# Performance work log

Hardware: AMD Instinct MI355X
Metric: run time of the kernel (lower is better)

Reference implementation:

```python
import jax, jax.numpy as jnp
import numpy as np


def log_g(x):
    # Appendix B.3 of 'Were RNNs All We Needed?'
    return jnp.where(x >= 0, jnp.log(jax.nn.relu(x) + 0.5), -jax.nn.softplus(-x))


def parallel_scan_log(log_a, log_b):
    # h[0] = b[0]; h[i] = a[i]*h[i-1] + b[i], computed in log space along axis 1
    log_a_star = jnp.cumsum(log_a, axis=1)
    log_x0_plus_b_star = jax.lax.cumlogsumexp(log_b - log_a_star, axis=1)
    return jnp.exp(log_a_star + log_x0_plus_b_star)


def setup_inputs() -> dict:
    key = jax.random.key(0)
    B, T, D = 8, 4096, 1024
    k1, k2, k3, k4, k5 = jax.random.split(key, 5)
    scale = 1.0 / np.sqrt(D)
    return {
        "h_prev_layer": jax.random.normal(k1, (B, T, D), dtype=jnp.float32),
        "W_z": jax.random.uniform(k2, (D, D), jnp.float32, -scale, scale),
        "b_z": jax.random.uniform(k3, (D,), jnp.float32, -scale, scale),
        "W_h": jax.random.uniform(k4, (D, D), jnp.float32, -scale, scale),
        "b_h": jax.random.uniform(k5, (D,), jnp.float32, -scale, scale),
    }


def reference(h_prev_layer, W_z, b_z, W_h, b_h):
    k = jnp.einsum('btd,ed->bte', h_prev_layer, W_z) + b_z          # linear_z
    tilde_h = jnp.einsum('btd,ed->bte', h_prev_layer, W_h) + b_h    # linear_h
    log_z = -jax.nn.softplus(-k)
    log_one_minus_z = -jax.nn.softplus(k)
    log_tilde_h = log_g(tilde_h)
    return parallel_scan_log(log_one_minus_z, log_z + log_tilde_h)
```

## Files before the change

### kernel.cpp

```cpp
#include <hip/hip_runtime.h>
#include <hip/hip_fp16.h>

typedef float f32x4 __attribute__((ext_vector_type(4)));
typedef __bf16 bf16x8 __attribute__((ext_vector_type(8)));
typedef unsigned int u32x4 __attribute__((ext_vector_type(4)));
typedef __attribute__((address_space(3))) const void* lds_cp;

#define BB_ 8
#define TT_ 4096
#define DD_ 1024
#define MM_ (BB_*TT_)
#define KK_ DD_

#define NCH 64
#define LCH (TT_/NCH)

static __device__ __forceinline__ unsigned short f2bf_rn(float f) {
  unsigned int u = __float_as_uint(f);
  u += 0x7FFFu + ((u >> 16) & 1u);
  return (unsigned short)(u >> 16);
}

__global__ void cvt_f32_bf16(const float4* __restrict__ src,
                             ushort4* __restrict__ dst, int n4) {
  int stride = gridDim.x * blockDim.x;
  for (int i = blockIdx.x * blockDim.x + threadIdx.x; i < n4; i += stride) {
    float4 v = src[i];
    ushort4 o;
    o.x = f2bf_rn(v.x); o.y = f2bf_rn(v.y);
    o.z = f2bf_rn(v.z); o.w = f2bf_rn(v.w);
    dst[i] = o;
  }
}

__global__ void cvt_w(const float4* __restrict__ Wz4,
                      const float4* __restrict__ Wh4,
                      ushort4* __restrict__ Wcat) {
  int flat = blockIdx.x * 256 + threadIdx.x;
  int mtx = flat >> 18;
  int j = flat & 262143;
  float4 v = (mtx ? Wh4 : Wz4)[j];
  int D = j >> 8;
  int kq = j & 255;
  int e = ((D >> 5) << 6) + (mtx << 5) + (D & 31);
  ushort4 o;
  o.x = f2bf_rn(v.x); o.y = f2bf_rn(v.y);
  o.z = f2bf_rn(v.z); o.w = f2bf_rn(v.w);
  Wcat[(size_t)e * 256 + kq] = o;
}

__device__ __forceinline__ void gload_lds16(const void* g, void* l) {
  __builtin_amdgcn_global_load_lds(
      (const __attribute__((address_space(1))) void*)g,
      (__attribute__((address_space(3))) void*)l, 16, 0, 0);
}

#define STA(q, nb_, kkh) gload_lds16(pXa + (q) * 65536 + (kkh), (nb_) + (q) * 8192 + wofs)
#define STB(q, nb_, kkh) gload_lds16(pWb + (q) * 65536 + (kkh), (nb_) + 32768 + (q) * 8192 + wofs)

#define DSR(dst, gp) \
  asm volatile("ds_read_b128 %0, %1" : "=&v"(dst) : "v"((lds_cp)(gp)))

#define RD_A(SET, base_, mh, sk_) do {                                      \
    DSR(SET[0], (base_) + rA7 + (mh) * 8192 + 0 * 2048 + (sk_));            \
    DSR(SET[1], (base_) + rA7 + (mh) * 8192 + 1 * 2048 + (sk_));            \
    DSR(SET[2], (base_) + rA7 + (mh) * 8192 + 2 * 2048 + (sk_));            \
    DSR(SET[3], (base_) + rA7 + (mh) * 8192 + 3 * 2048 + (sk_));            \
  } while (0)
#define RD_B(SET, base_, sk_) do {                                          \
    DSR(SET[0], (base_) + rB7 + 0 * 2048 + (sk_));                          \
    DSR(SET[1], (base_) + rB7 + 1 * 2048 + (sk_));                          \
    DSR(SET[2], (base_) + rB7 + 2 * 2048 + (sk_));                          \
    DSR(SET[3], (base_) + rB7 + 3 * 2048 + (sk_));                          \
  } while (0)

#define BC(x) __builtin_bit_cast(bf16x8, x)
#define MFMA16(ASET, BSET, mh) do {                                         \
    __builtin_amdgcn_s_setprio(1);                                          \
    _Pragma("unroll")                                                       \
    for (int ii = 0; ii < 4; ++ii)                                          \
      _Pragma("unroll")                                                     \
      for (int j = 0; j < 4; ++j)                                           \
        acc[(mh) * 4 + ii][j] = __builtin_amdgcn_mfma_f32_16x16x32_bf16(    \
            BC(ASET[ii]), BC(BSET[j]), acc[(mh) * 4 + ii][j], 0, 0, 0);     \
    __builtin_amdgcn_s_setprio(0);                                          \
  } while (0)

#define BAR() do { __builtin_amdgcn_s_barrier();                            \
                   __builtin_amdgcn_sched_barrier(0); } while (0)
#define SB()  __builtin_amdgcn_sched_barrier(0)
#define LGKM(n) do { asm volatile("s_waitcnt lgkmcnt(" #n ")" ::: "memory");\
                     SB(); } while (0)
#define VMW(n) asm volatile("s_waitcnt vmcnt(" #n ")" ::: "memory")

__global__ __launch_bounds__(512, 2) void gemm_fused(
    const unsigned short* __restrict__ Xb,
    const unsigned short* __restrict__ Wb,
    const float* __restrict__ bz, const float* __restrict__ bh,
    unsigned int* __restrict__ ZG,
    float* __restrict__ Pp, float* __restrict__ Qq)
{
  extern __shared__ __align__(16) char smem[];
  const int tid  = threadIdx.x;
  const int wave = tid >> 6;
  const int lane = tid & 63;
  const int wm = wave >> 2, wn = wave & 3;
  const int fr = lane & 15, kg = lane >> 4;

  int swz = (blockIdx.x & 7) * 128 + (blockIdx.x >> 3);
  const int m0 = (swz >> 3) * 256;
  const int e0 = (swz & 7) * 256;

  const int arow = tid >> 3;
  const int aslx = ((tid & 7) ^ (arow & 7)) * 8;
  const unsigned short* pXa = Xb + (size_t)(m0 + arow) * KK_ + aslx;
  const unsigned short* pWb = Wb + (size_t)(e0 + arow) * KK_ + aslx;
  const int wofs = wave * 1024;

  const int rA7 = (wm * 128 + fr) * 128;
  const int rB7 = 32768 + (wn * 64 + fr) * 128;
  const int fx = fr & 7;
  const int sk0 = (kg ^ fx) * 16;
  const int sk1 = sk0 ^ 64;

  f32x4 acc[8][4];
  #pragma unroll
  for (int i = 0; i < 8; i++)
    #pragma unroll
    for (int j = 0; j < 4; j++)
      acc[i][j] = (f32x4){0.f, 0.f, 0.f, 0.f};
  u32x4 aP[4], aQ[4], bk0[4], bk1[4];

  STA(0, smem, 0); STA(2, smem, 0); STB(0, smem, 0);
  STB(1, smem, 0); STB(2, smem, 0); STB(3, smem, 0);
  STA(1, smem, 0); STA(3, smem, 0);
  VMW(2);
  __builtin_amdgcn_s_barrier();
  SB();
  RD_A(aP, smem, 0, sk0);
  RD_B(bk0, smem, sk0);

  #pragma unroll 1
  for (int t = 0; t < 15; ++t) {
    const char* cb = smem + ((t & 1) << 16);
    char* nb = smem + (((t + 1) & 1) << 16);
    const int kn = (t + 1) * 64;
    VMW(0);
    BAR();
    RD_A(aQ, cb, 1, sk0);
    STA(0, nb, kn); STA(2, nb, kn); STB(0, nb, kn);
    LGKM(4);
    MFMA16(aP, bk0, 0);
    BAR();
    RD_A(aP, cb, 0, sk1);
    RD_B(bk1, cb, sk1);
    STB(1, nb, kn); STB(2, nb, kn); STB(3, nb, kn);
    LGKM(8);
    MFMA16(aQ, bk0, 1);
    BAR();
    RD_A(aQ, cb, 1, sk1);
    STA(1, nb, kn); STA(3, nb, kn);
    LGKM(4);
    MFMA16(aP, bk1, 0);
    VMW(2);
    BAR();
    RD_A(aP, nb, 0, sk0);
    RD_B(bk0, nb, sk0);
    LGKM(8);
    MFMA16(aQ, bk1, 1);
  }
  {
    const char* cb = smem + 65536;
    VMW(0);
    BAR();
    RD_A(aQ, cb, 1, sk0);
    LGKM(4);  MFMA16(aP, bk0, 0);
    BAR();
    RD_A(aP, cb, 0, sk1);
    RD_B(bk1, cb, sk1);
    LGKM(8);  MFMA16(aQ, bk0, 1);
    BAR();
    RD_A(aQ, cb, 1, sk1);
    LGKM(4);  MFMA16(aP, bk1, 0);
    BAR();
    LGKM(0);  MFMA16(aQ, bk1, 1);
  }
  __syncthreads();

  const int dw0 = (swz & 7) * 128 + wn * 32;
  const int t0 = m0 & 4095;
  const int bidx = m0 >> 12;

  float bzv[2], bhv[2];
  #pragma unroll
  for (int j = 0; j < 2; ++j) {
    bzv[j] = bz[dw0 + j * 16 + fr];
    bhv[j] = bh[dw0 + j * 16 + fr];
  }

  unsigned int* ew = (unsigned int*)(smem + wave * 9216);
  const int sub = lane & 7, rowr = lane >> 3;

  #pragma unroll
  for (int p = 0; p < 2; ++p) {
    float PP[2] = {1.f, 1.f}, QQ[2] = {0.f, 0.f};
    #pragma unroll
    for (int ii = 0; ii < 4; ++ii) {
      #pragma unroll
      for (int j = 0; j < 2; ++j) {
        float segP = 1.f, segQ = 0.f;
        #pragma unroll
        for (int r = 0; r < 4; ++r) {
          float kz = acc[p * 4 + ii][j][r] + bzv[j];
          float th = acc[p * 4 + ii][j + 2][r] + bhv[j];
          float z = 1.0f / (1.0f + __expf(-kz));
          float g = (th >= 0.0f) ? (th + 0.5f)
                                 : (1.0f / (1.0f + __expf(-th)));
          unsigned int pk =
              (unsigned int)__half_as_ushort(__float2half(z)) |
              ((unsigned int)__half_as_ushort(__float2half(g)) << 16);
          ew[(ii * 16 + kg * 4 + r) * 36 + j * 16 + fr] = pk;
          float aa = 1.f - z;
          segP *= aa;
          segQ = fmaf(aa, segQ, z * g);
        }
        float p1 = __shfl_down(segP, 16), q1 = __shfl_down(segQ, 16);
        segQ = fmaf(p1, segQ, q1); segP *= p1;
        float p2 = __shfl_down(segP, 32), q2 = __shfl_down(segQ, 32);
        segQ = fmaf(p2, segQ, q2); segP *= p2;
        QQ[j] = fmaf(segP, QQ[j], segQ);
        PP[j] *= segP;
      }
    }
    if (kg == 0) {
      const int cg = (t0 >> 6) + wm * 2 + p;
      #pragma unroll
      for (int j = 0; j < 2; ++j) {
        size_t po = ((size_t)bidx * NCH + cg) * DD_ + dw0 + j * 16 + fr;
        Pp[po] = PP[j];
        Qq[po] = QQ[j];
      }
    }
    #pragma unroll
    for (int q = 0; q < 8; ++q) {
      int rl = q * 8 + rowr;
      uint4 v = *reinterpret_cast<const uint4*>(&ew[rl * 36 + sub * 4]);
      size_t rg = (size_t)(m0 + wm * 128 + p * 64 + rl);
      *reinterpret_cast<uint4*>(&ZG[rg * DD_ + dw0 + sub * 4]) = v;
    }
  }
}

__global__ __launch_bounds__(256) void scan_combine(
    const float* __restrict__ P, const float* __restrict__ Q,
    float* __restrict__ H) {
  const int d = blockIdx.x * 256 + threadIdx.x;
  const int b = blockIdx.y;
  float h = 0.f;
  for (int c = 0; c < NCH; ++c) {
    size_t o = ((size_t)b * NCH + c) * DD_ + d;
    H[o] = h;
    h = fmaf(P[o], h, Q[o]);
  }
}

__global__ __launch_bounds__(256) void scan_apply(
    const uint4* __restrict__ ZG, const float4* __restrict__ H,
    float4* __restrict__ out) {
  const int d4 = threadIdx.x;
  const int c  = blockIdx.x;
  const int b  = blockIdx.y;
  float4 h = H[((size_t)b * NCH + c) * (DD_ / 4) + d4];
  size_t base = ((size_t)b * TT_ + (size_t)c * LCH) * (DD_ / 4) + d4;
  for (int t = 0; t < LCH; ++t) {
    uint4 w = ZG[base + (size_t)t * (DD_ / 4)];
    float z, g, a;
    z = __half2float(__ushort_as_half((unsigned short)(w.x & 0xffff)));
    g = __half2float(__ushort_as_half((unsigned short)(w.x >> 16)));
    a = 1.f - z; h.x = fmaf(a, h.x, z * g);
    z = __half2float(__ushort_as_half((unsigned short)(w.y & 0xffff)));
    g = __half2float(__ushort_as_half((unsigned short)(w.y >> 16)));
    a = 1.f - z; h.y = fmaf(a, h.y, z * g);
    z = __half2float(__ushort_as_half((unsigned short)(w.z & 0xffff)));
    g = __half2float(__ushort_as_half((unsigned short)(w.z >> 16)));
    a = 1.f - z; h.z = fmaf(a, h.z, z * g);
    z = __half2float(__ushort_as_half((unsigned short)(w.w & 0xffff)));
    g = __half2float(__ushort_as_half((unsigned short)(w.w >> 16)));
    a = 1.f - z; h.w = fmaf(a, h.w, z * g);
    out[base + (size_t)t * (DD_ / 4)] = h;
  }
}

extern "C" void kernel_launch(void* const* d_in, const int* in_sizes, int n_in,
                              void* d_out, int out_size, void* d_ws, size_t ws_size,
                              hipStream_t stream) {
  const float* X  = (const float*)d_in[0];
  const float* Wz = (const float*)d_in[1];
  const float* bz = (const float*)d_in[2];
  const float* Wh = (const float*)d_in[3];
  const float* bh = (const float*)d_in[4];
  float* out = (float*)d_out;

  const size_t szXb = (size_t)MM_ * DD_ * 2;
  const size_t szWb = (size_t)2 * DD_ * DD_ * 2;
  const size_t szZG = (size_t)MM_ * DD_ * 4;
  const size_t szPQ = (size_t)BB_ * NCH * DD_ * 4;

  char* ws = (char*)d_ws;
  unsigned short *Xb, *Wb;
  const size_t needA = szXb + szWb + szZG + 3 * szPQ;
  if (ws_size >= needA) {
    Xb = (unsigned short*)ws;              ws += szXb;
    Wb = (unsigned short*)ws;              ws += szWb;
  } else {
    Xb = (unsigned short*)d_out;
    Wb = (unsigned short*)((char*)d_out + szXb);
  }
  unsigned int* ZG = (unsigned int*)ws;  ws += szZG;
  float* P = (float*)ws;  ws += szPQ;
  float* Q = (float*)ws;  ws += szPQ;
  float* H = (float*)ws;

  cvt_f32_bf16<<<2048, 256, 0, stream>>>((const float4*)X, (ushort4*)Xb,
                                         (int)((size_t)MM_ * DD_ / 4));
  cvt_w<<<2048, 256, 0, stream>>>((const float4*)Wz, (const float4*)Wh,
                                  (ushort4*)Wb);
  gemm_fused<<<(MM_ / 256) * ((2 * DD_) / 256), 512, 131072, stream>>>(
      Xb, Wb, bz, bh, ZG, P, Q);

  scan_combine<<<dim3(4, BB_), 256, 0, stream>>>(P, Q, H);
  scan_apply<<<dim3(NCH, BB_), 256, 0, stream>>>((const uint4*)ZG,
                                                 (const float4*)H, (float4*)out);
}
```

Before: 263.4 us.

## Fuse fp32-to-bf16 conversion of X into the GEMM A-tile loads

Removes the separate X conversion kernel and its bf16 workspace buffer. The GEMM now loads fp32 X through registers, packs pairs to bf16 with v_cvt_pk_bf16_f32, and writes them to LDS, interleaved with the existing MFMA pipeline. This saves a full read and write pass over X in HBM. In exchange, the fp32 A reads per tile are twice as large and are re-read by each of the 8 N-blocks, and they use more VGPRs. The A path also loses the async global_load_lds path and the swizzled LDS write offset, which could hurt overlap or LDS layout correctness.

After: 297.6 us. 1.13x slower.

```diff
diff --git a/kernel.cpp b/kernel.cpp
--- a/kernel.cpp
+++ b/kernel.cpp
@@ -21,16 +21,10 @@
   return (unsigned short)(u >> 16);
 }
 
-__global__ void cvt_f32_bf16(const float4* __restrict__ src,
-                             ushort4* __restrict__ dst, int n4) {
-  int stride = gridDim.x * blockDim.x;
-  for (int i = blockIdx.x * blockDim.x + threadIdx.x; i < n4; i += stride) {
-    float4 v = src[i];
-    ushort4 o;
-    o.x = f2bf_rn(v.x); o.y = f2bf_rn(v.y);
-    o.z = f2bf_rn(v.z); o.w = f2bf_rn(v.w);
-    dst[i] = o;
-  }
+static __device__ __forceinline__ unsigned int cvtpk(float lo, float hi) {
+  unsigned int r;
+  asm("v_cvt_pk_bf16_f32 %0, %1, %2" : "=v"(r) : "v"(lo), "v"(hi));
+  return r;
 }
 
 __global__ void cvt_w(const float4* __restrict__ Wz4,
@@ -55,8 +49,18 @@
       (__attribute__((address_space(3))) void*)l, 16, 0, 0);
 }
 
-#define STA(q, nb_, kkh) gload_lds16(pXa + (q) * 65536 + (kkh), (nb_) + (q) * 8192 + wofs)
 #define STB(q, nb_, kkh) gload_lds16(pWb + (q) * 65536 + (kkh), (nb_) + 32768 + (q) * 8192 + wofs)
+
+#define LDA(VA, VB, q, kkh) do {                                            \
+    VA = *reinterpret_cast<const float4*>(pXa + (size_t)(q) * 65536 + (kkh));\
+    VB = *reinterpret_cast<const float4*>(pXa + (size_t)(q) * 65536 + (kkh) + 4);\
+  } while (0)
+#define CVW(VA, VB, q, nb_) do {                                            \
+    uint4 _o;                                                               \
+    _o.x = cvtpk(VA.x, VA.y); _o.y = cvtpk(VA.z, VA.w);                     \
+    _o.z = cvtpk(VB.x, VB.y); _o.w = cvtpk(VB.z, VB.w);                     \
+    *reinterpret_cast<uint4*>((nb_) + (q) * 8192 + (size_t)tid * 16) = _o;  \
+  } while (0)
 
 #define DSR(dst, gp) \
   asm volatile("ds_read_b128 %0, %1" : "=&v"(dst) : "v"((lds_cp)(gp)))
@@ -94,7 +98,7 @@
 #define VMW(n) asm volatile("s_waitcnt vmcnt(" #n ")" ::: "memory")
 
 __global__ __launch_bounds__(512, 2) void gemm_fused(
-    const unsigned short* __restrict__ Xb,
+    const float* __restrict__ Xf,
     const unsigned short* __restrict__ Wb,
     const float* __restrict__ bz, const float* __restrict__ bh,
     unsigned int* __restrict__ ZG,
@@ -113,7 +117,7 @@
 
   const int arow = tid >> 3;
   const int aslx = ((tid & 7) ^ (arow & 7)) * 8;
-  const unsigned short* pXa = Xb + (size_t)(m0 + arow) * KK_ + aslx;
+  const float* pXa = Xf + (size_t)(m0 + arow) * KK_ + aslx;
   const unsigned short* pWb = Wb + (size_t)(e0 + arow) * KK_ + aslx;
   const int wofs = wave * 1024;
 
@@ -130,11 +134,15 @@
     for (int j = 0; j < 4; j++)
       acc[i][j] = (f32x4){0.f, 0.f, 0.f, 0.f};
   u32x4 aP[4], aQ[4], bk0[4], bk1[4];
-
-  STA(0, smem, 0); STA(2, smem, 0); STB(0, smem, 0);
-  STB(1, smem, 0); STB(2, smem, 0); STB(3, smem, 0);
-  STA(1, smem, 0); STA(3, smem, 0);
-  VMW(2);
+  float4 xa0, xb0, xa1, xb1, xa2, xb2, xa3, xb3;
+
+  LDA(xa0, xb0, 0, 0); LDA(xa1, xb1, 1, 0);
+  LDA(xa2, xb2, 2, 0); LDA(xa3, xb3, 3, 0);
+  STB(0, smem, 0); STB(1, smem, 0); STB(2, smem, 0); STB(3, smem, 0);
+  CVW(xa0, xb0, 0, smem); CVW(xa1, xb1, 1, smem);
+  CVW(xa2, xb2, 2, smem); CVW(xa3, xb3, 3, smem);
+  VMW(0);
+  LGKM(0);
   __builtin_amdgcn_s_barrier();
   SB();
   RD_A(aP, smem, 0, sk0);
@@ -145,24 +153,26 @@
     const char* cb = smem + ((t & 1) << 16);
     char* nb = smem + (((t + 1) & 1) << 16);
     const int kn = (t + 1) * 64;
-    VMW(0);
     BAR();
     RD_A(aQ, cb, 1, sk0);
-    STA(0, nb, kn); STA(2, nb, kn); STB(0, nb, kn);
+    LDA(xa0, xb0, 0, kn); LDA(xa2, xb2, 2, kn);
+    STB(0, nb, kn);
     LGKM(4);
     MFMA16(aP, bk0, 0);
     BAR();
+    CVW(xa0, xb0, 0, nb); CVW(xa2, xb2, 2, nb);
     RD_A(aP, cb, 0, sk1);
     RD_B(bk1, cb, sk1);
+    LDA(xa1, xb1, 1, kn); LDA(xa3, xb3, 3, kn);
     STB(1, nb, kn); STB(2, nb, kn); STB(3, nb, kn);
     LGKM(8);
     MFMA16(aQ, bk0, 1);
     BAR();
+    CVW(xa1, xb1, 1, nb); CVW(xa3, xb3, 3, nb);
     RD_A(aQ, cb, 1, sk1);
-    STA(1, nb, kn); STA(3, nb, kn);
     LGKM(4);
     MFMA16(aP, bk1, 0);
-    VMW(2);
+    VMW(0);
     BAR();
     RD_A(aP, nb, 0, sk0);
     RD_B(bk0, nb, sk0);
@@ -171,7 +181,6 @@
   }
   {
     const char* cb = smem + 65536;
-    VMW(0);
     BAR();
     RD_A(aQ, cb, 1, sk0);
     LGKM(4);  MFMA16(aP, bk0, 0);
@@ -301,32 +310,21 @@
   const float* bh = (const float*)d_in[4];
   float* out = (float*)d_out;
 
-  const size_t szXb = (size_t)MM_ * DD_ * 2;
   const size_t szWb = (size_t)2 * DD_ * DD_ * 2;
   const size_t szZG = (size_t)MM_ * DD_ * 4;
   const size_t szPQ = (size_t)BB_ * NCH * DD_ * 4;
 
   char* ws = (char*)d_ws;
-  unsigned short *Xb, *Wb;
-  const size_t needA = szXb + szWb + szZG + 3 * szPQ;
-  if (ws_size >= needA) {
-    Xb = (unsigned short*)ws;              ws += szXb;
-    Wb = (unsigned short*)ws;              ws += szWb;
-  } else {
-    Xb = (unsigned short*)d_out;
-    Wb = (unsigned short*)((char*)d_out + szXb);
-  }
-  unsigned int* ZG = (unsigned int*)ws;  ws += szZG;
+  unsigned short* Wb = (unsigned short*)ws;  ws += szWb;
+  unsigned int* ZG = (unsigned int*)ws;      ws += szZG;
   float* P = (float*)ws;  ws += szPQ;
   float* Q = (float*)ws;  ws += szPQ;
   float* H = (float*)ws;
 
-  cvt_f32_bf16<<<2048, 256, 0, stream>>>((const float4*)X, (ushort4*)Xb,
-                                         (int)((size_t)MM_ * DD_ / 4));
   cvt_w<<<2048, 256, 0, stream>>>((const float4*)Wz, (const float4*)Wh,
                                   (ushort4*)Wb);
   gemm_fused<<<(MM_ / 256) * ((2 * DD_) / 256), 512, 131072, stream>>>(
-      Xb, Wb, bz, bh, ZG, P, Q);
+      X, Wb, bz, bh, ZG, P, Q);
 
   scan_combine<<<dim3(4, BB_), 256, 0, stream>>>(P, Q, H);
   scan_apply<<<dim3(NCH, BB_), 256, 0, stream>>>((const uint4*)ZG,
```
